# Optimization experiments

Measured on AMD Instinct MI355X. Metric: run time of the kernel, lower is better.

Reference implementation:

```python
import jax, jax.numpy as jnp
import numpy as np
import math

B, L = 512, 32768
NUM_C, NUM_D = 16, 8
RECIPTIVE, STRIDES = 512, 256
EPS = 1e-4


def setup_inputs() -> dict:
    key = jax.random.key(0)
    kx, kw = jax.random.split(key)
    x = jax.random.normal(kx, (B, L), dtype=jnp.float32)
    stdv = 1.0 / math.sqrt(RECIPTIVE)
    weight = jax.random.uniform(kw, (NUM_C, NUM_D, RECIPTIVE), dtype=jnp.float32,
                                minval=-stdv, maxval=stdv)
    return {"x": x, "weight": weight}


def reference(x, weight):
    # x: [B, L], weight: [C, D, R]
    Lx = x.shape[1]
    # sigma = (W W^T + eps I)^{-1} per capsule, [C, D, D]
    wc = jnp.einsum('cdr,cer->cde', weight, weight)
    sigma = jnp.linalg.inv(wc + EPS * jnp.eye(NUM_D, dtype=weight.dtype))
    # circular sliding windows: [W, R] index map (wraparound matches torch.cat branch)
    starts = jnp.arange(0, Lx, STRIDES)
    idx = (starts[:, None] + jnp.arange(RECIPTIVE)[None, :]) % Lx
    windows = x[:, idx]                                   # [B, W, R]
    proj = jnp.einsum('cdr,bwr->bwcd', weight, windows)    # [B, W, C, D]
    q = jnp.einsum('bwcd,cde,bwce->bwc', proj, sigma, proj)  # quadratic form
    return jnp.mean(jnp.sqrt(q), axis=1)                   # [B, C]
```

## Files before the change

kernel.cpp:

```cpp
#include <hip/hip_runtime.h>

#define NUM_C  16
#define NUM_D  8
#define RECEPT 512
#define NWIN   128
#define LROW   32768
#define EPS_V  1e-4f

#define XBYTES 66048

typedef __attribute__((ext_vector_type(8))) short short8;
typedef __attribute__((ext_vector_type(4))) float f32x4;

__device__ __forceinline__ unsigned short f2bf(float f) {
    unsigned int u = __builtin_bit_cast(unsigned int, f);
    u += 0x7fffu + ((u >> 16) & 1u);
    return (unsigned short)(u >> 16);
}

__device__ __forceinline__ int xsw(int a) { return a ^ (((a >> 9) & 7) << 4); }

__global__ void prep_kernel(const float* __restrict__ weight,
                            unsigned short* __restrict__ wfrag,
                            float* __restrict__ out) {
    __shared__ float Wc[NUM_D * RECEPT];
    __shared__ float G[NUM_D][NUM_D];
    __shared__ float Lm[NUM_D][NUM_D];
    const int c = blockIdx.x;
    const int t = threadIdx.x;

    #pragma unroll
    for (int i = 0; i < 8; ++i) out[c * 64 + t + i * 1024] = 0.f;

    const float* wsrc = weight + (size_t)c * NUM_D * RECEPT;
    for (int i = t; i < NUM_D * RECEPT; i += 64) Wc[i] = wsrc[i];
    __syncthreads();
    {
        int d = t >> 3, e = t & 7;
        const float4* wd4 = reinterpret_cast<const float4*>(&Wc[d * RECEPT]);
        const float4* we4 = reinterpret_cast<const float4*>(&Wc[e * RECEPT]);
        float s = 0.f;
        #pragma unroll 4
        for (int r4 = 0; r4 < RECEPT / 4; ++r4) {
            float4 a = wd4[r4], bb = we4[r4];
            s += a.x * bb.x + a.y * bb.y + a.z * bb.z + a.w * bb.w;
        }
        if (d == e) s += EPS_V;
        G[d][e] = s;
    }
    __syncthreads();
    if (t == 0) {
        for (int i = 0; i < NUM_D; ++i) {
            float diag = G[i][i];
            for (int k = 0; k < i; ++k) diag -= Lm[i][k] * Lm[i][k];
            float di = sqrtf(diag);
            Lm[i][i] = di;
            float inv = 1.f / di;
            for (int jj = i + 1; jj < NUM_D; ++jj) {
                float s = G[jj][i];
                for (int k = 0; k < i; ++k) s -= Lm[jj][k] * Lm[i][k];
                Lm[jj][i] = s * inv;
            }
        }
    }
    __syncthreads();
    for (int r = t; r < RECEPT; r += 64) {
        float y[NUM_D];
        for (int d = 0; d < NUM_D; ++d) {
            float s = Wc[d * RECEPT + r];
            for (int k = 0; k < d; ++k) s -= Lm[d][k] * y[k];
            y[d] = s / Lm[d][d];
        }
        const int kk = r >> 5;
        const int g  = (r >> 3) & 3;
        const int j  = r & 7;
        for (int d = 0; d < NUM_D; ++d) {
            int cd = c * NUM_D + d;
            int ntile = cd >> 4;
            int nl = cd & 15;
            int lane = g * 16 + nl;
            int idx = (((ntile * 16 + kk) * 64) + lane) * 8 + j;
            wfrag[idx] = f2bf(y[d]);
        }
    }
}

__global__ __launch_bounds__(512, 4) void main_kernel(
        const float* __restrict__ x,
        const unsigned short* __restrict__ wfrag,
        float* __restrict__ out) {
    extern __shared__ char lds[];
    const int b = blockIdx.x;
    const int t = threadIdx.x;
    const int lane = t & 63;
    const int wv = t >> 6;
    const int wmb = (wv & 1) * 64;
    const int wnb = (wv >> 1) * 32;

    const float4* xrow4 = reinterpret_cast<const float4*>(x + (size_t)b * LROW);

    #pragma unroll
    for (int i = 0; i < 16; ++i) {
        int f4 = i * 512 + t;
        float4 v = xrow4[f4];
        ushort4 h;
        h.x = f2bf(v.x); h.y = f2bf(v.y); h.z = f2bf(v.z); h.w = f2bf(v.w);
        *reinterpret_cast<ushort4*>(lds + xsw(f4 * 8)) = h;
    }
    if (t < 64) {
        float4 v = xrow4[t];
        ushort4 h;
        h.x = f2bf(v.x); h.y = f2bf(v.y); h.z = f2bf(v.z); h.w = f2bf(v.w);
        *reinterpret_cast<ushort4*>(lds + xsw(65536 + t * 8)) = h;
    }

    f32x4 acc[4][2];
    #pragma unroll
    for (int mi = 0; mi < 4; ++mi)
        #pragma unroll
        for (int ni = 0; ni < 2; ++ni)
            acc[mi][ni] = (f32x4){0.f, 0.f, 0.f, 0.f};

    const int rl = lane & 15;
    const int gl = lane >> 4;

    const int nt0 = wnb >> 4;
    const unsigned short* bb0 = wfrag + ((size_t)(nt0 * 16) * 64 + lane) * 8;
    const unsigned short* bb1 = wfrag + ((size_t)((nt0 + 1) * 16) * 64 + lane) * 8;

    __syncthreads();

    #pragma unroll 2
    for (int kk = 0; kk < 16; ++kk) {
        short8 af[4], bf0, bf1;
        const int kb = kk * 64 + gl * 16;
        #pragma unroll
        for (int mi = 0; mi < 4; ++mi) {
            int w = wmb + mi * 16 + rl;
            af[mi] = *reinterpret_cast<const short8*>(lds + xsw(w * 512 + kb));
        }
        bf0 = *reinterpret_cast<const short8*>(bb0 + kk * 512);
        bf1 = *reinterpret_cast<const short8*>(bb1 + kk * 512);
        #pragma unroll
        for (int mi = 0; mi < 4; ++mi) {
            acc[mi][0] = __builtin_amdgcn_mfma_f32_16x16x32_bf16(af[mi], bf0, acc[mi][0], 0, 0, 0);
            acc[mi][1] = __builtin_amdgcn_mfma_f32_16x16x32_bf16(af[mi], bf1, acc[mi][1], 0, 0, 0);
        }
    }

    #pragma unroll
    for (int ni = 0; ni < 2; ++ni) {
        float s = 0.f;
        #pragma unroll
        for (int mi = 0; mi < 4; ++mi) {
            #pragma unroll
            for (int r = 0; r < 4; ++r) {
                float p = acc[mi][ni][r];
                float q = p * p;
                q += __shfl_xor(q, 1);
                q += __shfl_xor(q, 2);
                q += __shfl_xor(q, 4);
                s += sqrtf(q);
            }
        }
        s += __shfl_xor(s, 16);
        s += __shfl_xor(s, 32);
        if (lane < 16 && (lane & 7) == 0) {
            int c = (wnb + ni * 16 + lane) >> 3;
            atomicAdd(&out[b * NUM_C + c], s * (1.0f / 128.0f));
        }
    }
}

extern "C" void kernel_launch(void* const* d_in, const int* in_sizes, int n_in,
                              void* d_out, int out_size, void* d_ws, size_t ws_size,
                              hipStream_t stream) {
    (void)in_sizes; (void)n_in; (void)ws_size; (void)out_size;
    const float* x      = (const float*)d_in[0];
    const float* weight = (const float*)d_in[1];
    float* out = (float*)d_out;
    unsigned short* wfrag = (unsigned short*)d_ws;

    prep_kernel<<<16, 64, 0, stream>>>(weight, wfrag, out);

    hipFuncSetAttribute(reinterpret_cast<const void*>(main_kernel),
                        hipFuncAttributeMaxDynamicSharedMemorySize, XBYTES);
    main_kernel<<<512, 512, XBYTES, stream>>>(x, wfrag, out);
}
```

Baseline: 36.83 us.

## Stage weight fragments through double-buffered LDS and widen prep kernel

The main kernel now copies the bf16 weight fragments into shared memory in four quarters, using two buffers. Each next quarter is prefetched into registers while the MFMA loop runs on the current one, which replaces per-iteration global loads of B fragments with LDS reads. This adds 64KB of LDS per block, lowers the launch-bounds occupancy hint from 4 to 2, and adds a barrier per quarter. The prep kernel also moves from 64 to 256 threads with vectorized weight loads.

```diff
diff --git a/kernel.cpp b/kernel.cpp
--- a/kernel.cpp
+++ b/kernel.cpp
@@ -7,7 +7,9 @@
 #define LROW   32768
 #define EPS_V  1e-4f
 
-#define XBYTES 66048
+#define XBYTES  66048
+#define WQBYTES 32768
+#define LDS_TOTAL (XBYTES + 2 * WQBYTES)
 
 typedef __attribute__((ext_vector_type(8))) short short8;
 typedef __attribute__((ext_vector_type(4))) float f32x4;
@@ -29,13 +31,17 @@
     const int c = blockIdx.x;
     const int t = threadIdx.x;
 
-    #pragma unroll
-    for (int i = 0; i < 8; ++i) out[c * 64 + t + i * 1024] = 0.f;
-
-    const float* wsrc = weight + (size_t)c * NUM_D * RECEPT;
-    for (int i = t; i < NUM_D * RECEPT; i += 64) Wc[i] = wsrc[i];
-    __syncthreads();
-    {
+    out[c * 256 + t] = 0.f;
+    out[c * 256 + t + 4096] = 0.f;
+
+    const float4* wsrc4 = reinterpret_cast<const float4*>(
+        weight + (size_t)c * NUM_D * RECEPT);
+    float4* Wc4 = reinterpret_cast<float4*>(Wc);
+    #pragma unroll
+    for (int i = 0; i < 4; ++i) Wc4[t + i * 256] = wsrc4[t + i * 256];
+    __syncthreads();
+
+    if (t < 64) {
         int d = t >> 3, e = t & 7;
         const float4* wd4 = reinterpret_cast<const float4*>(&Wc[d * RECEPT]);
         const float4* we4 = reinterpret_cast<const float4*>(&Wc[e * RECEPT]);
@@ -64,7 +70,7 @@
         }
     }
     __syncthreads();
-    for (int r = t; r < RECEPT; r += 64) {
+    for (int r = t; r < RECEPT; r += 256) {
         float y[NUM_D];
         for (int d = 0; d < NUM_D; ++d) {
             float s = Wc[d * RECEPT + r];
@@ -85,7 +91,7 @@
     }
 }
 
-__global__ __launch_bounds__(512, 4) void main_kernel(
+__global__ __launch_bounds__(512, 2) void main_kernel(
         const float* __restrict__ x,
         const unsigned short* __restrict__ wfrag,
         float* __restrict__ out) {
@@ -96,8 +102,19 @@
     const int wv = t >> 6;
     const int wmb = (wv & 1) * 64;
     const int wnb = (wv >> 1) * 32;
+    const int nt0 = wnb >> 4;
+    const int rl = lane & 15;
+    const int gl = lane >> 4;
 
     const float4* xrow4 = reinterpret_cast<const float4*>(x + (size_t)b * LROW);
+    const float4* wsrc = reinterpret_cast<const float4*>(wfrag);
+
+    float4 wreg[4];
+    #pragma unroll
+    for (int i = 0; i < 4; ++i) {
+        int d = i * 512 + t;
+        wreg[i] = wsrc[((d >> 8) << 10) + (d & 255)];
+    }
 
     #pragma unroll
     for (int i = 0; i < 16; ++i) {
@@ -113,6 +130,12 @@
         h.x = f2bf(v.x); h.y = f2bf(v.y); h.z = f2bf(v.z); h.w = f2bf(v.w);
         *reinterpret_cast<ushort4*>(lds + xsw(65536 + t * 8)) = h;
     }
+    {
+        float4* wd = reinterpret_cast<float4*>(lds + XBYTES);
+        #pragma unroll
+        for (int i = 0; i < 4; ++i) wd[i * 512 + t] = wreg[i];
+    }
+    __syncthreads();
 
     f32x4 acc[4][2];
     #pragma unroll
@@ -121,31 +144,40 @@
         for (int ni = 0; ni < 2; ++ni)
             acc[mi][ni] = (f32x4){0.f, 0.f, 0.f, 0.f};
 
-    const int rl = lane & 15;
-    const int gl = lane >> 4;
-
-    const int nt0 = wnb >> 4;
-    const unsigned short* bb0 = wfrag + ((size_t)(nt0 * 16) * 64 + lane) * 8;
-    const unsigned short* bb1 = wfrag + ((size_t)((nt0 + 1) * 16) * 64 + lane) * 8;
-
-    __syncthreads();
-
-    #pragma unroll 2
-    for (int kk = 0; kk < 16; ++kk) {
-        short8 af[4], bf0, bf1;
-        const int kb = kk * 64 + gl * 16;
-        #pragma unroll
-        for (int mi = 0; mi < 4; ++mi) {
-            int w = wmb + mi * 16 + rl;
-            af[mi] = *reinterpret_cast<const short8*>(lds + xsw(w * 512 + kb));
-        }
-        bf0 = *reinterpret_cast<const short8*>(bb0 + kk * 512);
-        bf1 = *reinterpret_cast<const short8*>(bb1 + kk * 512);
-        #pragma unroll
-        for (int mi = 0; mi < 4; ++mi) {
-            acc[mi][0] = __builtin_amdgcn_mfma_f32_16x16x32_bf16(af[mi], bf0, acc[mi][0], 0, 0, 0);
-            acc[mi][1] = __builtin_amdgcn_mfma_f32_16x16x32_bf16(af[mi], bf1, acc[mi][1], 0, 0, 0);
-        }
+    #pragma unroll
+    for (int q = 0; q < 4; ++q) {
+        if (q < 3) {
+            #pragma unroll
+            for (int i = 0; i < 4; ++i) {
+                int d = i * 512 + t;
+                wreg[i] = wsrc[((d >> 8) << 10) + (q + 1) * 256 + (d & 255)];
+            }
+        }
+        const char* wb = lds + XBYTES + (q & 1) * WQBYTES;
+        #pragma unroll
+        for (int kkq = 0; kkq < 4; ++kkq) {
+            const int kk = q * 4 + kkq;
+            short8 af[4], bf0, bf1;
+            const int kb = kk * 64 + gl * 16;
+            #pragma unroll
+            for (int mi = 0; mi < 4; ++mi) {
+                int w = wmb + mi * 16 + rl;
+                af[mi] = *reinterpret_cast<const short8*>(lds + xsw(w * 512 + kb));
+            }
+            bf0 = *reinterpret_cast<const short8*>(wb + ((nt0 * 4 + kkq) * 64 + lane) * 16);
+            bf1 = *reinterpret_cast<const short8*>(wb + (((nt0 + 1) * 4 + kkq) * 64 + lane) * 16);
+            #pragma unroll
+            for (int mi = 0; mi < 4; ++mi) {
+                acc[mi][0] = __builtin_amdgcn_mfma_f32_16x16x32_bf16(af[mi], bf0, acc[mi][0], 0, 0, 0);
+                acc[mi][1] = __builtin_amdgcn_mfma_f32_16x16x32_bf16(af[mi], bf1, acc[mi][1], 0, 0, 0);
+            }
+        }
+        if (q < 3) {
+            float4* wd = reinterpret_cast<float4*>(lds + XBYTES + ((q + 1) & 1) * WQBYTES);
+            #pragma unroll
+            for (int i = 0; i < 4; ++i) wd[i * 512 + t] = wreg[i];
+        }
+        __syncthreads();
     }
 
     #pragma unroll
@@ -156,11 +188,11 @@
             #pragma unroll
             for (int r = 0; r < 4; ++r) {
                 float p = acc[mi][ni][r];
-                float q = p * p;
-                q += __shfl_xor(q, 1);
-                q += __shfl_xor(q, 2);
-                q += __shfl_xor(q, 4);
-                s += sqrtf(q);
+                float qq = p * p;
+                qq += __shfl_xor(qq, 1);
+                qq += __shfl_xor(qq, 2);
+                qq += __shfl_xor(qq, 4);
+                s += sqrtf(qq);
             }
         }
         s += __shfl_xor(s, 16);
@@ -181,9 +213,9 @@
     float* out = (float*)d_out;
     unsigned short* wfrag = (unsigned short*)d_ws;
 
-    prep_kernel<<<16, 64, 0, stream>>>(weight, wfrag, out);
+    prep_kernel<<<16, 256, 0, stream>>>(weight, wfrag, out);
 
     hipFuncSetAttribute(reinterpret_cast<const void*>(main_kernel),
-                        hipFuncAttributeMaxDynamicSharedMemorySize, XBYTES);
-    main_kernel<<<512, 512, XBYTES, stream>>>(x, wfrag, out);
-}
+                        hipFuncAttributeMaxDynamicSharedMemorySize, LDS_TOTAL);
+    main_kernel<<<512, 512, LDS_TOTAL, stream>>>(x, wfrag, out);
+}
```

New measurement: 49.19 us. +33.6%, slower.
